# Kernel tuning notes

Hardware: AMD Instinct MI355X
Metric: run time of the kernel (lower is better)

Reference implementation:

```python
import jax, jax.numpy as jnp
import numpy as np

SEQ_LEN = 20
NFEATURES = 812
HID = 400
VAR = 811
B = 8192


def setup_inputs() -> dict:
    key = jax.random.key(0)
    ks = jax.random.split(key, 12)
    sd = 1.0 / np.sqrt(HID)
    sl = 1.0 / np.sqrt(HID)  # lstm stdv per torch (1/sqrt(hidden))
    return {
        "values": jax.random.normal(ks[0], (B, SEQ_LEN, NFEATURES), jnp.float32),
        "masks": jnp.round(jax.random.uniform(ks[1], (B, SEQ_LEN), jnp.float32)),
        "deltas": jax.random.uniform(ks[2], (B, SEQ_LEN), jnp.float32),
        "W_decay": jax.random.uniform(ks[3], (HID, NFEATURES), jnp.float32, -sd, sd),
        "b_decay": jax.random.uniform(ks[4], (HID,), jnp.float32, -sd, sd),
        "W_reg": jax.random.uniform(ks[5], (1, HID), jnp.float32, -sd, sd),
        "b_reg": jax.random.uniform(ks[6], (1,), jnp.float32, -sd, sd),
        "W_ih": jax.random.uniform(ks[7], (4 * HID, NFEATURES + 1), jnp.float32, -sl, sl),
        "W_hh": jax.random.uniform(ks[8], (4 * HID, HID), jnp.float32, -sl, sl),
        "b_ih": jax.random.uniform(ks[9], (4 * HID,), jnp.float32, -sl, sl),
        "b_hh": jax.random.uniform(ks[10], (4 * HID,), jnp.float32, -sl, sl),
    }


def reference(values, masks, deltas, W_decay, b_decay, W_reg, b_reg, W_ih, W_hh, b_ih, b_hh):
    # direct == 'forward' (time runs t = 0..SEQ_LEN-1)
    batch = values.shape[0]
    # deltas.unsqueeze(2).repeat(1,1,NF) followed by F.linear(d, W) ==
    # d[:, None] * W.sum(axis=1) + b  (d is a per-sample scalar repeated)
    w_sum = jnp.sum(W_decay, axis=1)  # [HID]

    def step(carry, xs):
        h, c, loss = carry
        x, m, d = xs  # x: [B, NF], m: [B], d: [B]
        gamma = jnp.exp(-jax.nn.relu(d[:, None] * w_sum[None, :] + b_decay))  # [B, HID]
        h = h * gamma
        x_h = (h @ W_reg.T + b_reg)[:, 0]  # [B]
        x_var = x[:, VAR] * m + (1.0 - m) * x_h
        x = x.at[:, VAR].set(x_var)
        step_loss = jnp.sum(jnp.abs(x_var - x_h) * m) / (jnp.sum(m) + 1e-5)
        inp = jnp.concatenate([x, m[:, None]], axis=1)  # [B, NF+1]
        gates = inp @ W_ih.T + b_ih + h @ W_hh.T + b_hh  # [B, 4*HID]
        i_g, f_g, g_g, o_g = jnp.split(gates, 4, axis=1)
        c = jax.nn.sigmoid(f_g) * c + jax.nn.sigmoid(i_g) * jnp.tanh(g_g)
        h = jax.nn.sigmoid(o_g) * jnp.tanh(c)
        return (h, c, loss + step_loss), x_var

    h0 = jnp.zeros((batch, HID), values.dtype)
    c0 = jnp.zeros((batch, HID), values.dtype)
    xs = (jnp.swapaxes(values, 0, 1), masks.T, deltas.T)  # time-major [T, B, ...]
    (h, c, x_loss), imps = jax.lax.scan(step, (h0, c0, jnp.float32(0.0)), xs)
    imputations = imps.T  # [B, SEQ_LEN]
    return x_loss / SEQ_LEN, imputations
```

## Files before the change

### kernel.cpp

```cpp
#include <hip/hip_runtime.h>
#include <math.h>

#define B 8192
#define T 20
#define NF 812
#define HID 400
#define NG 1600
#define NGP 1664
#define VARI 811
#define KP 832
#define KPB (KP * 2)
#define KPC 13
#define KH 448
#define KHB (KH * 2)
#define KHC 7
#define BM 128
#define BN 128
#define MROWS (B * T)
#define PRE_BLOCKS (13 * (MROWS / BM))
#define STEP_BLOCKS (13 * (B / BM))
#define GT_STRIDE 68

typedef __attribute__((ext_vector_type(8))) short short8;
typedef __attribute__((ext_vector_type(4))) short short4v;
typedef __attribute__((ext_vector_type(4))) unsigned short ushort4v;
typedef __attribute__((ext_vector_type(4))) float floatx4;

__device__ inline short f2bf(float f) {
    union { float f; unsigned u; } v; v.f = f;
    unsigned r = v.u + 0x7FFF + ((v.u >> 16) & 1);
    return (short)(r >> 16);
}
__device__ inline float bf2f(unsigned short s) {
    union { float f; unsigned u; } v; v.u = ((unsigned)s) << 16;
    return v.f;
}
__device__ inline void glds16(const void* g, void* l) {
    __builtin_amdgcn_global_load_lds(
        (const __attribute__((address_space(1))) void*)g,
        (__attribute__((address_space(3))) void*)l, 16, 0, 0);
}
__device__ inline float sigm(float x) { return 1.f / (1.f + expf(-x)); }

__device__ inline void gemm_mainloop(const char* __restrict__ Ag,
                                     const char* __restrict__ Bg,
                                     short* As, short* Bs,
                                     int kc_count, int kbytes_row,
                                     int wave, int lane,
                                     floatx4 acc[4][4]) {
    int wm = wave & 1, wn = wave >> 1;
    int q = lane >> 4;
    int mr = lane & 15;
    int rsub = lane >> 3;
    int cix = ((lane & 7) - rsub) & 7;

    for (int kc = 0; kc < kc_count; kc++) {
        int kbyte = kc * 128;
#pragma unroll
        for (int i = 0; i < 4; i++) {
            int r0 = wave * 32 + i * 8;
            int r = r0 + rsub;
            glds16(Ag + (size_t)r * kbytes_row + kbyte + cix * 16,
                   (char*)As + r0 * 128);
            glds16(Bg + (size_t)r * kbytes_row + kbyte + cix * 16,
                   (char*)Bs + r0 * 128);
        }
        __syncthreads();
        const short8* Av = (const short8*)As;
        const short8* Bv = (const short8*)Bs;
#pragma unroll
        for (int kk = 0; kk < 2; kk++) {
            short8 a[4], b[4];
#pragma unroll
            for (int f = 0; f < 4; f++) {
                int arow = wm * 64 + f * 16 + mr;
                a[f] = Av[arow * 8 + ((kk * 4 + q + mr) & 7)];
                int brow = wn * 64 + f * 16 + mr;
                b[f] = Bv[brow * 8 + ((kk * 4 + q + mr) & 7)];
            }
#pragma unroll
            for (int f = 0; f < 4; f++)
#pragma unroll
                for (int g = 0; g < 4; g++)
                    acc[f][g] = __builtin_amdgcn_mfma_f32_16x16x32_bf16(
                        a[f], b[g], acc[f][g], 0, 0, 0);
        }
        __syncthreads();
    }
}

__global__ void prep_kernel(const float* __restrict__ W_decay,
                            const float* __restrict__ masks,
                            float* __restrict__ wsum,
                            float* __restrict__ den) {
    int blk = blockIdx.x;
    int lane = threadIdx.x;
    if (blk < HID) {
        float s = 0.f;
        for (int k = lane; k < NF; k += 64) s += W_decay[blk * NF + k];
        for (int o = 32; o; o >>= 1) s += __shfl_down(s, o);
        if (lane == 0) wsum[blk] = s;
    } else {
        int t = blk - HID;
        if (t < T) {
            float s = 0.f;
            for (int b = lane; b < B; b += 64) s += masks[b * T + t];
            for (int o = 32; o; o >>= 1) s += __shfl_down(s, o);
            if (lane == 0) den[t] = s;
        }
    }
}

__global__ void conv_inp(const float* __restrict__ values,
                         const float* __restrict__ masks,
                         short* __restrict__ Inpb) {
    int row = blockIdx.x;
    int t = threadIdx.x;
    if (t >= 208) return;
    short4v o;
    if (t < 202) {
        const float4* src = (const float4*)(values + (size_t)row * NF + 4 * t);
        float4 v = *src;
        o.x = f2bf(v.x); o.y = f2bf(v.y); o.z = f2bf(v.z); o.w = f2bf(v.w);
    } else if (t == 202) {
        const float4* src = (const float4*)(values + (size_t)row * NF + 808);
        float4 v = *src;
        o.x = f2bf(v.x); o.y = f2bf(v.y); o.z = f2bf(v.z); o.w = 0;
    } else if (t == 203) {
        o.x = f2bf(masks[row]); o.y = 0; o.z = 0; o.w = 0;
    } else {
        o.x = o.y = o.z = o.w = 0;
    }
    *(short4v*)(Inpb + (size_t)row * KP + 4 * t) = o;
}

__global__ void conv_wih(const float* __restrict__ W_ih,
                         const float* __restrict__ b_ih,
                         const float* __restrict__ b_hh,
                         short* __restrict__ Wihb,
                         float* __restrict__ w811r,
                         float* __restrict__ biasr) {
    int rp = blockIdx.x;
    int t = threadIdx.x;
    if (rp < NG) {
        int j = rp >> 2, g = rp & 3;
        int r = g * HID + j;
        if (t < 208) {
            short4v o;
#pragma unroll
            for (int i = 0; i < 4; i++) {
                int k = 4 * t + i;
                float v = (k < NF + 1) ? W_ih[(size_t)r * (NF + 1) + k] : 0.f;
                ((short*)&o)[i] = f2bf(v);
            }
            *(short4v*)(Wihb + (size_t)rp * KP + 4 * t) = o;
        } else if (t == 255) {
            w811r[rp] = W_ih[(size_t)r * (NF + 1) + VARI];
            biasr[rp] = b_ih[r] + b_hh[r];
        }
    } else {
        if (t < 208) {
            short4v o; o.x = o.y = o.z = o.w = 0;
            *(short4v*)(Wihb + (size_t)rp * KP + 4 * t) = o;
        } else if (t == 255) {
            w811r[rp] = 0.f;
            biasr[rp] = 0.f;
        }
    }
}

__global__ void conv_whh(const float* __restrict__ W_hh,
                         short* __restrict__ Whhb) {
    int rp = blockIdx.x;
    int t = threadIdx.x;
    if (t >= 112) return;
    short4v o; o.x = o.y = o.z = o.w = 0;
    if (rp < NG) {
        int j = rp >> 2, g = rp & 3;
        int r = g * HID + j;
#pragma unroll
        for (int i = 0; i < 4; i++) {
            int k = 4 * t + i;
            float v = (k < HID) ? W_hh[(size_t)r * HID + k] : 0.f;
            ((short*)&o)[i] = f2bf(v);
        }
    }
    *(short4v*)(Whhb + (size_t)rp * KH + 4 * t) = o;
}

__global__ __launch_bounds__(256, 2)
void pre_gemm(const short* __restrict__ Inpb,
              const short* __restrict__ Wihb,
              const float* __restrict__ biasr,
              short* __restrict__ preb) {
    __shared__ __align__(16) short As[BM * 64];
    __shared__ __align__(16) short Bs[BN * 64];
    int lin = blockIdx.x;
    int swz = (lin & 7) * (PRE_BLOCKS / 8) + (lin >> 3);
    int ty = swz / 13, tx = swz - ty * 13;
    int row0 = ty * BM, n0 = tx * BN;
    int tid = threadIdx.x, lane = tid & 63, wave = tid >> 6;

    floatx4 acc[4][4] = {};
    gemm_mainloop((const char*)(Inpb + (size_t)row0 * KP),
                  (const char*)(Wihb + (size_t)n0 * KP),
                  As, Bs, KPC, KPB, wave, lane, acc);

    int wm = wave & 1, wn = wave >> 1, q = lane >> 4, mr = lane & 15;
#pragma unroll
    for (int g = 0; g < 4; g++) {
        int gn = n0 + wn * 64 + g * 16 + mr;
        if (gn < NG) {
            float bia = biasr[gn];
#pragma unroll
            for (int f = 0; f < 4; f++)
#pragma unroll
                for (int r = 0; r < 4; r++) {
                    int m = wm * 64 + f * 16 + q * 4 + r;
                    preb[(size_t)(row0 + m) * NG + gn] = f2bf(acc[f][g][r] + bia);
                }
        }
    }
}

__global__ __launch_bounds__(256)
void decay_impute(int t,
                  const float* __restrict__ values,
                  const float* __restrict__ masks,
                  const float* __restrict__ deltas,
                  const float* __restrict__ b_decay,
                  const float* __restrict__ W_reg,
                  const float* __restrict__ b_reg,
                  const float* __restrict__ wsum,
                  const float* __restrict__ h,
                  short* __restrict__ hbf,
                  float* __restrict__ xvar,
                  float* __restrict__ num,
                  float* __restrict__ out_imp) {
    __shared__ float red[4];
    int wave = threadIdx.x >> 6;
    int lane = threadIdx.x & 63;
    float lnum = 0.f;
#pragma unroll
    for (int i = 0; i < 2; i++) {
        int b = (blockIdx.x * 4 + wave) * 2 + i;
        float d = deltas[b * T + t];
        float m = masks[b * T + t];
        float dot = 0.f;
        for (int j = lane; j < HID; j += 64) {
            float g = expf(-fmaxf(fmaf(d, wsum[j], b_decay[j]), 0.f));
            float hv = h[(size_t)b * HID + j] * g;
            hbf[(size_t)b * KH + j] = f2bf(hv);
            dot = fmaf(hv, W_reg[j], dot);
        }
        if (lane < KH - HID) hbf[(size_t)b * KH + HID + lane] = 0;
        for (int o = 32; o; o >>= 1) dot += __shfl_down(dot, o);
        if (lane == 0) {
            float x_h = dot + b_reg[0];
            float xv = values[(size_t)(b * T + t) * NF + VARI];
            float x_var = xv * m + (1.f - m) * x_h;
            out_imp[b * T + t] = x_var;
            xvar[b] = x_var;
            if (m != 0.f) lnum += fabsf(x_var - x_h);
        }
    }
    if (lane == 0) red[wave] = lnum;
    __syncthreads();
    if (threadIdx.x == 0)
        atomicAdd(&num[t], red[0] + red[1] + red[2] + red[3]);
}

__global__ __launch_bounds__(256, 2)
void step_gemm(int t,
               const short* __restrict__ hbf,
               const short* __restrict__ Whhb,
               const short* __restrict__ preb,
               const float* __restrict__ w811r,
               const float* __restrict__ xvar,
               float* __restrict__ c,
               float* __restrict__ h_out) {
    __shared__ __align__(16) char smem[BM * GT_STRIDE * 4];
    short* As = (short*)smem;
    short* Bs = (short*)(smem + 16384);
    float* gt = (float*)smem;
    int lin = blockIdx.x;
    int swz = (lin & 7) * (STEP_BLOCKS / 8) + (lin >> 3);
    int ty = swz / 13, tx = swz - ty * 13;
    int b0 = ty * BM, n0 = tx * BN;
    int tid = threadIdx.x, lane = tid & 63, wave = tid >> 6;

    floatx4 acc[4][4] = {};
    gemm_mainloop((const char*)(hbf + (size_t)b0 * KH),
                  (const char*)(Whhb + (size_t)n0 * KH),
                  As, Bs, KHC, KHB, wave, lane, acc);

    int wm = wave & 1, wn = wave >> 1, q = lane >> 4, mr = lane & 15;
    int jl = tid & 15, bb0 = tid >> 4;
#pragma unroll
    for (int nh = 0; nh < 2; nh++) {
        __syncthreads();
        if (wn == nh) {
#pragma unroll
            for (int f = 0; f < 4; f++)
#pragma unroll
                for (int g = 0; g < 4; g++)
#pragma unroll
                    for (int r = 0; r < 4; r++)
                        gt[(wm * 64 + f * 16 + q * 4 + r) * GT_STRIDE +
                           g * 16 + mr] = acc[f][g][r];
        }
        __syncthreads();
        int rpb = n0 + nh * 64 + jl * 4;
        int j = rpb >> 2;
        float w0 = w811r[rpb + 0];
        float w1 = w811r[rpb + 1];
        float w2 = w811r[rpb + 2];
        float w3 = w811r[rpb + 3];
        bool inb = (rpb < NG);
        bool jok = (j < HID);
#pragma unroll
        for (int i = 0; i < 8; i++) {
            int bb = bb0 + i * 16;
            int b = b0 + bb;
            float xv = xvar[b];
            float4 gv = *(const float4*)&gt[bb * GT_STRIDE + jl * 4];
            float pi = 0.f, pf = 0.f, pg = 0.f, po = 0.f;
            if (inb) {
                ushort4v pv = *(const ushort4v*)(preb +
                    ((size_t)b * T + t) * NG + rpb);
                pi = bf2f(pv.x); pf = bf2f(pv.y);
                pg = bf2f(pv.z); po = bf2f(pv.w);
            }
            float gi = gv.x + pi + xv * w0;
            float gf = gv.y + pf + xv * w1;
            float gg = gv.z + pg + xv * w2;
            float go = gv.w + po + xv * w3;
            if (jok) {
                size_t idx = (size_t)b * HID + j;
                float cn = sigm(gf) * c[idx] + sigm(gi) * tanhf(gg);
                c[idx] = cn;
                h_out[idx] = sigm(go) * tanhf(cn);
            }
        }
    }
}

__global__ void finalize_kernel(const float* __restrict__ num,
                                const float* __restrict__ den,
                                float* __restrict__ out) {
    if (threadIdx.x == 0) {
        float s = 0.f;
        for (int t = 0; t < T; t++) s += num[t] / (den[t] + 1e-5f);
        out[0] = s / (float)T;
    }
}

extern "C" void kernel_launch(void* const* d_in, const int* in_sizes, int n_in,
                              void* d_out, int out_size, void* d_ws, size_t ws_size,
                              hipStream_t stream) {
    const float* values  = (const float*)d_in[0];
    const float* masks   = (const float*)d_in[1];
    const float* deltas  = (const float*)d_in[2];
    const float* W_decay = (const float*)d_in[3];
    const float* b_decay = (const float*)d_in[4];
    const float* W_reg   = (const float*)d_in[5];
    const float* b_reg   = (const float*)d_in[6];
    const float* W_ih    = (const float*)d_in[7];
    const float* W_hh    = (const float*)d_in[8];
    const float* b_ih    = (const float*)d_in[9];
    const float* b_hh    = (const float*)d_in[10];
    float* out = (float*)d_out;

    char* p = (char*)d_ws;
    auto alloc = [&](size_t bytes) { char* r = p; p += (bytes + 255) & ~(size_t)255; return r; };
    const size_t BH = (size_t)B * HID;
    float* h0    = (float*)alloc(BH * 4);
    float* c     = (float*)alloc(BH * 4);
    float* h1    = (float*)alloc(BH * 4);
    short* hbf   = (short*)alloc((size_t)B * KH * 2);
    float* xvar  = (float*)alloc(B * 4);
    float* wsum  = (float*)alloc(HID * 4);
    float* w811r = (float*)alloc(NGP * 4);
    float* biasr = (float*)alloc(NGP * 4);
    float* num   = (float*)alloc(32 * 4);
    float* den   = (float*)alloc(32 * 4);
    short* Wihb  = (short*)alloc((size_t)NGP * KP * 2);
    short* Whhb  = (short*)alloc((size_t)NGP * KH * 2);
    short* Inpb  = (short*)alloc((size_t)MROWS * KP * 2);
    short* preb  = (short*)alloc((size_t)MROWS * NG * 2);

    hipMemsetAsync(h0, 0, 2 * BH * 4, stream);
    hipMemsetAsync(num, 0, 32 * 4, stream);

    prep_kernel<<<HID + T, 64, 0, stream>>>(W_decay, masks, wsum, den);
    conv_wih<<<NGP, 256, 0, stream>>>(W_ih, b_ih, b_hh, Wihb, w811r, biasr);
    conv_whh<<<NGP, 128, 0, stream>>>(W_hh, Whhb);
    conv_inp<<<MROWS, 256, 0, stream>>>(values, masks, Inpb);
    pre_gemm<<<PRE_BLOCKS, 256, 0, stream>>>(Inpb, Wihb, biasr, preb);
    for (int t = 0; t < T; t++) {
        float* hin  = (t & 1) ? h1 : h0;
        float* hout = (t & 1) ? h0 : h1;
        decay_impute<<<B / 8, 256, 0, stream>>>(
            t, values, masks, deltas, b_decay, W_reg, b_reg, wsum,
            hin, hbf, xvar, num, out + 1);
        step_gemm<<<STEP_BLOCKS, 256, 0, stream>>>(
            t, hbf, Whhb, preb, w811r, xvar, c, hout);
    }
    finalize_kernel<<<1, 64, 0, stream>>>(num, den, out);
}
```

Measured before the change: 2.643 ms.

## Fuse decay and regression dot into step GEMM epilogue, drop fp32 h buffers

Moves the next step's gamma decay, bf16 conversion of the decayed hidden state and the W_reg partial dot into the LSTM step GEMM epilogue. Partial dots are accumulated with atomics into a per-batch x_h buffer, so the per-step imputation kernel shrinks to a tiny per-sample kernel. This removes the fp32 h write and re-read and the separate decay pass each step. In exchange it adds global atomics, extra epilogue arithmetic in the GEMM and ping-pong bf16 hidden buffers.

```diff
diff --git a/kernel.cpp b/kernel.cpp
--- a/kernel.cpp
+++ b/kernel.cpp
@@ -224,47 +224,27 @@
 }
 
 __global__ __launch_bounds__(256)
-void decay_impute(int t,
-                  const float* __restrict__ values,
-                  const float* __restrict__ masks,
-                  const float* __restrict__ deltas,
-                  const float* __restrict__ b_decay,
-                  const float* __restrict__ W_reg,
-                  const float* __restrict__ b_reg,
-                  const float* __restrict__ wsum,
-                  const float* __restrict__ h,
-                  short* __restrict__ hbf,
-                  float* __restrict__ xvar,
-                  float* __restrict__ num,
-                  float* __restrict__ out_imp) {
+void xvar_kernel(int t,
+                 const float* __restrict__ values,
+                 const float* __restrict__ masks,
+                 const float* __restrict__ b_reg,
+                 float* __restrict__ xh,
+                 float* __restrict__ xvar,
+                 float* __restrict__ num,
+                 float* __restrict__ out_imp) {
     __shared__ float red[4];
-    int wave = threadIdx.x >> 6;
-    int lane = threadIdx.x & 63;
-    float lnum = 0.f;
-#pragma unroll
-    for (int i = 0; i < 2; i++) {
-        int b = (blockIdx.x * 4 + wave) * 2 + i;
-        float d = deltas[b * T + t];
-        float m = masks[b * T + t];
-        float dot = 0.f;
-        for (int j = lane; j < HID; j += 64) {
-            float g = expf(-fmaxf(fmaf(d, wsum[j], b_decay[j]), 0.f));
-            float hv = h[(size_t)b * HID + j] * g;
-            hbf[(size_t)b * KH + j] = f2bf(hv);
-            dot = fmaf(hv, W_reg[j], dot);
-        }
-        if (lane < KH - HID) hbf[(size_t)b * KH + HID + lane] = 0;
-        for (int o = 32; o; o >>= 1) dot += __shfl_down(dot, o);
-        if (lane == 0) {
-            float x_h = dot + b_reg[0];
-            float xv = values[(size_t)(b * T + t) * NF + VARI];
-            float x_var = xv * m + (1.f - m) * x_h;
-            out_imp[b * T + t] = x_var;
-            xvar[b] = x_var;
-            if (m != 0.f) lnum += fabsf(x_var - x_h);
-        }
-    }
-    if (lane == 0) red[wave] = lnum;
+    int b = blockIdx.x * 256 + threadIdx.x;
+    float x_h = xh[b] + b_reg[0];
+    xh[b] = 0.f;
+    float m = masks[b * T + t];
+    float xv = values[(size_t)(b * T + t) * NF + VARI];
+    float x_var = xv * m + (1.f - m) * x_h;
+    out_imp[b * T + t] = x_var;
+    xvar[b] = x_var;
+    float l = (m != 0.f) ? fabsf(x_var - x_h) : 0.f;
+    for (int o = 32; o; o >>= 1) l += __shfl_down(l, o);
+    int lane = threadIdx.x & 63, wave = threadIdx.x >> 6;
+    if (lane == 0) red[wave] = l;
     __syncthreads();
     if (threadIdx.x == 0)
         atomicAdd(&num[t], red[0] + red[1] + red[2] + red[3]);
@@ -272,13 +252,18 @@
 
 __global__ __launch_bounds__(256, 2)
 void step_gemm(int t,
-               const short* __restrict__ hbf,
+               const short* __restrict__ hbf_in,
+               short* __restrict__ hbf_out,
                const short* __restrict__ Whhb,
                const short* __restrict__ preb,
                const float* __restrict__ w811r,
                const float* __restrict__ xvar,
+               const float* __restrict__ deltas,
+               const float* __restrict__ b_decay,
+               const float* __restrict__ wsum,
+               const float* __restrict__ W_reg,
                float* __restrict__ c,
-               float* __restrict__ h_out) {
+               float* __restrict__ xh_next) {
     __shared__ __align__(16) char smem[BM * GT_STRIDE * 4];
     short* As = (short*)smem;
     short* Bs = (short*)(smem + 16384);
@@ -290,12 +275,17 @@
     int tid = threadIdx.x, lane = tid & 63, wave = tid >> 6;
 
     floatx4 acc[4][4] = {};
-    gemm_mainloop((const char*)(hbf + (size_t)b0 * KH),
+    gemm_mainloop((const char*)(hbf_in + (size_t)b0 * KH),
                   (const char*)(Whhb + (size_t)n0 * KH),
                   As, Bs, KHC, KHB, wave, lane, acc);
 
     int wm = wave & 1, wn = wave >> 1, q = lane >> 4, mr = lane & 15;
     int jl = tid & 15, bb0 = tid >> 4;
+    bool dec = (t + 1 < T);
+    float xhp[8];
+#pragma unroll
+    for (int i = 0; i < 8; i++) xhp[i] = 0.f;
+
 #pragma unroll
     for (int nh = 0; nh < 2; nh++) {
         __syncthreads();
@@ -318,6 +308,9 @@
         float w3 = w811r[rpb + 3];
         bool inb = (rpb < NG);
         bool jok = (j < HID);
+        float wsj = jok ? wsum[j] : 0.f;
+        float bdj = jok ? b_decay[j] : 0.f;
+        float wrj = jok ? W_reg[j] : 0.f;
 #pragma unroll
         for (int i = 0; i < 8; i++) {
             int bb = bb0 + i * 16;
@@ -339,7 +332,28 @@
                 size_t idx = (size_t)b * HID + j;
                 float cn = sigm(gf) * c[idx] + sigm(gi) * tanhf(gg);
                 c[idx] = cn;
-                h_out[idx] = sigm(go) * tanhf(cn);
+                float hn = sigm(go) * tanhf(cn);
+                if (dec) {
+                    float d = deltas[b * T + t + 1];
+                    float gam = expf(-fmaxf(fmaf(d, wsj, bdj), 0.f));
+                    float hv = hn * gam;
+                    hbf_out[(size_t)b * KH + j] = f2bf(hv);
+                    xhp[i] += hv * wrj;
+                }
+            }
+        }
+    }
+    if (dec) {
+#pragma unroll
+        for (int i = 0; i < 8; i++) {
+            float s = xhp[i];
+            s += __shfl_xor(s, 1);
+            s += __shfl_xor(s, 2);
+            s += __shfl_xor(s, 4);
+            s += __shfl_xor(s, 8);
+            if (jl == 0) {
+                int b = b0 + bb0 + i * 16;
+                atomicAdd(&xh_next[b], s);
             }
         }
     }
@@ -374,11 +388,12 @@
     char* p = (char*)d_ws;
     auto alloc = [&](size_t bytes) { char* r = p; p += (bytes + 255) & ~(size_t)255; return r; };
     const size_t BH = (size_t)B * HID;
-    float* h0    = (float*)alloc(BH * 4);
     float* c     = (float*)alloc(BH * 4);
-    float* h1    = (float*)alloc(BH * 4);
-    short* hbf   = (short*)alloc((size_t)B * KH * 2);
+    short* hbf0  = (short*)alloc((size_t)B * KH * 2);
+    short* hbf1  = (short*)alloc((size_t)B * KH * 2);
     float* xvar  = (float*)alloc(B * 4);
+    float* xh0   = (float*)alloc(B * 4);
+    float* xh1   = (float*)alloc(B * 4);
     float* wsum  = (float*)alloc(HID * 4);
     float* w811r = (float*)alloc(NGP * 4);
     float* biasr = (float*)alloc(NGP * 4);
@@ -389,7 +404,10 @@
     short* Inpb  = (short*)alloc((size_t)MROWS * KP * 2);
     short* preb  = (short*)alloc((size_t)MROWS * NG * 2);
 
-    hipMemsetAsync(h0, 0, 2 * BH * 4, stream);
+    hipMemsetAsync(c, 0, BH * 4, stream);
+    hipMemsetAsync(hbf0, 0, (size_t)B * KH * 2, stream);
+    hipMemsetAsync(hbf1, 0, (size_t)B * KH * 2, stream);
+    hipMemsetAsync(xh0, 0, (size_t)2 * B * 4, stream);
     hipMemsetAsync(num, 0, 32 * 4, stream);
 
     prep_kernel<<<HID + T, 64, 0, stream>>>(W_decay, masks, wsum, den);
@@ -398,13 +416,15 @@
     conv_inp<<<MROWS, 256, 0, stream>>>(values, masks, Inpb);
     pre_gemm<<<PRE_BLOCKS, 256, 0, stream>>>(Inpb, Wihb, biasr, preb);
     for (int t = 0; t < T; t++) {
-        float* hin  = (t & 1) ? h1 : h0;
-        float* hout = (t & 1) ? h0 : h1;
-        decay_impute<<<B / 8, 256, 0, stream>>>(
-            t, values, masks, deltas, b_decay, W_reg, b_reg, wsum,
-            hin, hbf, xvar, num, out + 1);
+        short* hin  = (t & 1) ? hbf1 : hbf0;
+        short* hout = (t & 1) ? hbf0 : hbf1;
+        float* xh_cur  = (t & 1) ? xh1 : xh0;
+        float* xh_next = (t & 1) ? xh0 : xh1;
+        xvar_kernel<<<B / 256, 256, 0, stream>>>(
+            t, values, masks, b_reg, xh_cur, xvar, num, out + 1);
         step_gemm<<<STEP_BLOCKS, 256, 0, stream>>>(
-            t, hbf, Whhb, preb, w811r, xvar, c, hout);
+            t, hin, hout, Whhb, preb, w811r, xvar,
+            deltas, b_decay, wsum, W_reg, c, xh_next);
     }
     finalize_kernel<<<1, 64, 0, stream>>>(num, den, out);
 }
```

New measurement: 2.376 ms. -10.1%, faster.
